# Performance work log

Measured on AMD Instinct MI355X. Metric: run time of the kernel, lower is better.

The kernel has to match this reference:

```python
import jax, jax.numpy as jnp
import numpy as np

W, H = 1920, 1080
WEIGHT = 0.2          # self.weight
CONT_W = 0.1          # continuity_weight
RANK_M = 1e-4         # ranking_margin
CONT_M = 1e-4         # continuity_margin
SAMPLE_RATIO = 0.25
R = 3                 # knn_crop_radius
PAD_VAL = -1000000.0


def setup_inputs() -> dict:
    key = jax.random.key(0)
    k1, k2, k3 = jax.random.split(key, 3)
    return {
        "target_depths": jax.random.uniform(k1, (1, H * W), dtype=jnp.float32) * 100.0,
        "render_depths": jax.random.uniform(k2, (H * W,), dtype=jnp.float32) * 100.0,
        "valid_mask": jax.random.randint(k3, (1, H * W, 1), 0, 2, dtype=jnp.int32),
        "width": W,
        "height": H,
    }


def _sample_depth_loss_indices(depths, width, height, valid_mask, n_samples,
                               rank_patch_size, r, key):
    win = 2 * r + 1                      # 7
    top_n = int(0.3 * win * win + 1)     # 15
    ks = jax.random.split(key, 5)
    sy = jax.random.randint(ks[0], (n_samples, 1), 0, height - rank_patch_size)
    sx = jax.random.randint(ks[1], (n_samples, 1), 0, width - rank_patch_size)
    sy = sy + jax.random.randint(ks[2], (n_samples, 2), 0, rank_patch_size)
    sx = sx + jax.random.randint(ks[3], (n_samples, 2), 0, rank_patch_size)
    sample_idx = sy * width + sx                               # (n, 2)
    sampled_depth = depths[0][sample_idx]                      # (n, 2)

    padded = jnp.pad(depths.reshape(height, width), r, constant_values=PAD_VAL)
    dy = jnp.repeat(jnp.arange(win), win)                      # (49,) row offsets
    dx = jnp.tile(jnp.arange(win), win)                        # (49,) col offsets
    # padded coords: (y - r + dy) + r == y + dy
    py = sy[..., None] + dy                                    # (n, 2, 49)
    px = sx[..., None] + dx
    depth_crops = padded[py, px]                               # (n, 2, 49)

    sorted_crop_idx = jnp.argsort(jnp.abs(depth_crops - sampled_depth[..., None]), axis=-1)
    nbr_sample = jax.random.randint(ks[4], (n_samples, 2, 1), 1, top_n)
    rel = jnp.take_along_axis(sorted_crop_idx, nbr_sample, axis=-1)[..., 0]  # (n, 2)
    ny = sy - r + rel // win
    nx = sx - r + rel % win
    neighbours_idx = ny * width + nx                           # (n, 2)

    vm = valid_mask[0].astype(bool)                            # (H*W, C)
    samples_mask = vm[sample_idx].any(-1).all(-1)              # (n,)
    neighbours_mask = vm[neighbours_idx].any(-1).all(-1)
    full_mask = samples_mask & neighbours_mask

    # per-pair descending sort by sampled target depth
    order = jnp.argsort(-sampled_depth, axis=-1)
    s_sorted = jnp.take_along_axis(sample_idx, order, axis=-1)
    n_sorted = jnp.take_along_axis(neighbours_idx, order, axis=-1)
    idx4 = jnp.concatenate([s_sorted, n_sorted], axis=-1)      # (n, 4)
    return idx4, full_mask


def reference(target_depths, render_depths, valid_mask, width, height):
    n_samples = int(width * height * SAMPLE_RATIO)
    rank_patch_size = width // 8
    idx4, mask = _sample_depth_loss_indices(
        target_depths, width, height, valid_mask, n_samples, rank_patch_size,
        R, jax.random.key(42))
    d = render_depths[idx4].reshape(-1, 2, 2)                  # (n, 2, 2)
    rank = jnp.maximum(d[:, 0, 0] - d[:, 0, 1] + RANK_M, 0.0)  # (n,)
    cont = jnp.maximum(jnp.abs(d[:, 0, :] - d[:, 1, :]) - CONT_M, 0.0)  # (n, 2)
    # masked means == torch's boolean filtering followed by .mean()
    m = mask.astype(rank.dtype)
    denom = jnp.maximum(m.sum(), 1.0)
    rank_mean = (rank * m).sum() / denom
    cont_mean = (cont * m[:, None]).sum() / (denom * 2.0)
    return jnp.stack([WEIGHT * rank_mean, WEIGHT * CONT_W * cont_mean])
```

## Files before the change

kernel.cpp:

```cpp
#include <hip/hip_runtime.h>
#include <stdint.h>


#define IMG_W 1920
#define IMG_H 1080
#define N_PIX (IMG_W * IMG_H)
#define N_SAMP 518400
#define PAD_VAL (-1000000.0f)

struct Keys { uint32_t k[5][2][2]; };

static __host__ __device__ inline void tf2x32(uint32_t k0, uint32_t k1,
                                              uint32_t x0, uint32_t x1,
                                              uint32_t& o0, uint32_t& o1)
{
  const uint32_t ks2 = k0 ^ k1 ^ 0x1BD11BDAu;
  x0 += k0; x1 += k1;
#define TFR(r) { x0 += x1; x1 = (x1 << (r)) | (x1 >> (32 - (r))); x1 ^= x0; }
  TFR(13) TFR(15) TFR(26) TFR(6)
  x0 += k1;  x1 += ks2 + 1u;
  TFR(17) TFR(29) TFR(16) TFR(24)
  x0 += ks2; x1 += k0 + 2u;
  TFR(13) TFR(15) TFR(26) TFR(6)
  x0 += k0;  x1 += k1 + 3u;
  TFR(17) TFR(29) TFR(16) TFR(24)
  x0 += k1;  x1 += ks2 + 4u;
  TFR(13) TFR(15) TFR(26) TFR(6)
  x0 += ks2; x1 += k0 + 5u;
#undef TFR
  o0 = x0; o1 = x1;
}

__device__ __forceinline__ uint32_t jrbits(const uint32_t kk[2], uint32_t f)
{
  uint32_t a, b;
  tf2x32(kk[0], kk[1], 0u, f, a, b);
  return a ^ b;
}

__device__ __forceinline__ uint32_t jrandint(const Keys& K, int r, uint32_t f,
                                             uint32_t span)
{
  const uint32_t hi = jrbits(K.k[r][0], f);
  const uint32_t lo = jrbits(K.k[r][1], f);
  uint32_t m = 65536u % span;
  m = (m * m) % span;
  return ((hi % span) * m + (lo % span)) % span;
}

static void compute_keys(Keys& K)
{
  uint32_t ks[5][2];
  for (uint32_t t = 0; t < 5; t++) {
    uint32_t a, b; tf2x32(0u, 42u, 0u, t, a, b);
    ks[t][0] = a; ks[t][1] = b;
  }
  for (int r = 0; r < 5; r++) {
    uint32_t a, b;
    tf2x32(ks[r][0], ks[r][1], 0u, 0u, a, b); K.k[r][0][0] = a; K.k[r][0][1] = b;
    tf2x32(ks[r][0], ks[r][1], 0u, 1u, a, b); K.k[r][1][0] = a; K.k[r][1][1] = b;
  }
}

__device__ __forceinline__ bool validat(const unsigned long long* __restrict__ vb,
                                        const int* __restrict__ vm, uint32_t idx)
{
  if (vb) return ((vb[idx >> 6] >> (idx & 63u)) & 1ull) != 0ull;
  return vm[idx] != 0;
}

__global__ __launch_bounds__(256) void gs_bitpack(
    const int* __restrict__ vmask,
    unsigned long long* __restrict__ vbits)
{
  const uint32_t gid = blockIdx.x * 256u + threadIdx.x;
  const unsigned long long ball = __ballot(vmask[gid] != 0);
  if ((threadIdx.x & 63u) == 0) vbits[gid >> 6] = ball;
}

__device__ __forceinline__ int crop_neighbor(const float* __restrict__ tgt,
                                             int sy, int sx, float sd,
                                             uint32_t nbr)
{
  float v[7][8];
  const bool interior = (sy >= 3) && (sy <= IMG_H - 4) &&
                        (sx >= 3) && (sx <= IMG_W - 5);
  if (interior) {
    const float* p = tgt + (sy - 3) * IMG_W + (sx - 3);
#pragma unroll
    for (int r = 0; r < 7; r++)
      __builtin_memcpy(&v[r][0], p + r * IMG_W, 32);
  } else {
#pragma unroll
    for (int r = 0; r < 7; r++) {
      const int yy = sy - 3 + r;
      const bool rok = (yy >= 0) && (yy < IMG_H);
#pragma unroll
      for (int c = 0; c < 8; c++) {
        const int xx = sx - 3 + c;
        const bool okc = rok && (c < 7) && (xx >= 0) && (xx < IMG_W);
        v[r][c] = okc ? tgt[yy * IMG_W + xx] : PAD_VAL;
      }
    }
  }
  __builtin_amdgcn_sched_barrier(0);

  uint32_t arr[15];
#pragma unroll
  for (int t = 0; t < 15; t++) arr[t] = 0xFFFFFFFFu;

#pragma unroll
  for (int r = 0; r < 7; r++) {
#pragma unroll
    for (int c = 0; c < 7; c++) {
      const int q = r * 7 + c;
      uint32_t key = (__float_as_uint(v[r][c] - sd) & 0x7FFFFFC0u) | (uint32_t)q;
      const int depth = (q + 1 < 15) ? (q + 1) : 15;
#pragma unroll
      for (int t = 0; t < 15; t++) {
        if (t < depth) {
          const uint32_t lo = min(key, arr[t]);
          const uint32_t hi = max(key, arr[t]);
          arr[t] = lo; key = hi;
        }
      }
    }
  }

  uint32_t relkey = 0;
#pragma unroll
  for (int t = 1; t < 15; t++)
    if ((uint32_t)t == nbr) relkey = arr[t];
  const uint32_t rel = relkey & 63u;
  const int ny = sy - 3 + (int)(rel / 7u);
  const int nx = sx - 3 + (int)(rel % 7u);
  return ny * IMG_W + nx;
}

__global__ __launch_bounds__(256, 2) void gs_fused(
    const float* __restrict__ tgt,
    const float* __restrict__ rnd,
    const int*   __restrict__ vmask,
    const unsigned long long* __restrict__ vbits,
    float* __restrict__ acc,
    Keys K)
{
  __shared__ unsigned long long ent[512];
  __shared__ float    res_sd[1024];
  __shared__ int      res_ni[1024];
  __shared__ uint32_t scnt[8];
  __shared__ float    partial[12];

  const uint32_t tid  = threadIdx.x;
  const uint32_t lane = tid & 63u;
  const uint32_t wave = tid >> 6;

  unsigned long long e[2];
  bool ok[2];
#pragma unroll
  for (int h = 0; h < 2; h++) {
    const uint32_t ui = blockIdx.x * 512u + (uint32_t)h * 256u + tid;
    bool o = false;
    unsigned long long ee = 0;
    if (ui < N_SAMP) {
      const uint32_t syb = jrandint(K, 0, ui, 840u);
      const uint32_t sxb = jrandint(K, 1, ui, 1680u);
      const uint32_t sy0 = syb + jrandint(K, 2, 2u * ui,      240u);
      const uint32_t sy1 = syb + jrandint(K, 2, 2u * ui + 1u, 240u);
      const uint32_t sx0 = sxb + jrandint(K, 3, 2u * ui,      240u);
      const uint32_t sx1 = sxb + jrandint(K, 3, 2u * ui + 1u, 240u);
      o = validat(vbits, vmask, sy0 * IMG_W + sx0) &&
          validat(vbits, vmask, sy1 * IMG_W + sx1);
      ee = ((unsigned long long)ui  << 44) |
           ((unsigned long long)sy0 << 33) | ((unsigned long long)sx0 << 22) |
           ((unsigned long long)sy1 << 11) |  (unsigned long long)sx1;
    }
    ok[h] = o; e[h] = ee;
  }

  const unsigned long long b0 = __ballot(ok[0]);
  const unsigned long long b1 = __ballot(ok[1]);
  if (lane == 0) {
    scnt[wave]     = (uint32_t)__popcll(b0);
    scnt[4 + wave] = (uint32_t)__popcll(b1);
  }
  __syncthreads();

  uint32_t base0 = 0, sum0 = 0, base1 = 0, nsurv = 0;
#pragma unroll
  for (uint32_t w = 0; w < 4; w++) {
    if (w < wave) { base0 += scnt[w]; base1 += scnt[4 + w]; }
    sum0  += scnt[w];
    nsurv += scnt[w] + scnt[4 + w];
  }
  base1 += sum0;

  if (ok[0]) ent[base0 + (uint32_t)__popcll(b0 & ((1ull << lane) - 1ull))] = e[0];
  if (ok[1]) ent[base1 + (uint32_t)__popcll(b1 & ((1ull << lane) - 1ull))] = e[1];
  __syncthreads();

  for (uint32_t t = tid; t < 2u * nsurv; t += 256u) {
    const unsigned long long ee = ent[t >> 1];
    const int jj = (int)(t & 1u);
    const uint32_t eui = (uint32_t)(ee >> 44);
    const int sy = jj ? (int)((ee >> 11) & 2047u) : (int)((ee >> 33) & 2047u);
    const int sx = jj ? (int)( ee        & 2047u) : (int)((ee >> 22) & 2047u);

    const float sd = tgt[sy * IMG_W + sx];
    const uint32_t nbr = 1u + jrandint(K, 4, 2u * eui + (uint32_t)jj, 14u);
    const int nidx = crop_neighbor(tgt, sy, sx, sd, nbr);
    res_sd[t] = sd;
    res_ni[t] = validat(vbits, vmask, (uint32_t)nidx) ? nidx : -1;
  }
  __syncthreads();

  float rank_c = 0.f, cont_c = 0.f, cnt_c = 0.f;
  for (uint32_t s = tid; s < nsurv; s += 256u) {
    const int n0 = res_ni[2u * s], n1 = res_ni[2u * s + 1u];
    if ((n0 >= 0) && (n1 >= 0)) {
      const unsigned long long ee = ent[s];
      const int esy0 = (int)((ee >> 33) & 2047u), esx0 = (int)((ee >> 22) & 2047u);
      const int esy1 = (int)((ee >> 11) & 2047u), esx1 = (int)( ee        & 2047u);
      const float r0 = rnd[esy0 * IMG_W + esx0];
      const float r1 = rnd[esy1 * IMG_W + esx1];
      const float q0 = rnd[n0], q1 = rnd[n1];
      const float sd0 = res_sd[2u * s], sd1 = res_sd[2u * s + 1u];
      const bool keep = sd0 >= sd1;
      const float ra = keep ? r0 : r1;
      const float rb = keep ? r1 : r0;
      rank_c += fmaxf(ra - rb + 1e-4f, 0.f);
      cont_c += fmaxf(fabsf(r0 - q0) - 1e-4f, 0.f)
              + fmaxf(fabsf(r1 - q1) - 1e-4f, 0.f);
      cnt_c  += 1.f;
    }
  }

#pragma unroll
  for (int off = 32; off > 0; off >>= 1) {
    rank_c += __shfl_down(rank_c, off);
    cont_c += __shfl_down(cont_c, off);
    cnt_c  += __shfl_down(cnt_c, off);
  }
  if (lane == 0) {
    partial[wave * 3 + 0] = rank_c;
    partial[wave * 3 + 1] = cont_c;
    partial[wave * 3 + 2] = cnt_c;
  }
  __syncthreads();
  if (tid < 3) {
    const float s = partial[tid] + partial[3 + tid] +
                    partial[6 + tid] + partial[9 + tid];
    atomicAdd(acc + tid, s);
  }
}

__global__ void gs_finalize(const float* __restrict__ acc, float* __restrict__ out)
{
  const float denom = fmaxf(acc[2], 1.0f);
  out[0] = 0.2f * (acc[0] / denom);
  out[1] = 0.2f * 0.1f * (acc[1] / (denom * 2.0f));
}

extern "C" void kernel_launch(void* const* d_in, const int* in_sizes, int n_in,
                              void* d_out, int out_size, void* d_ws, size_t ws_size,
                              hipStream_t stream)
{
  (void)in_sizes; (void)n_in; (void)out_size;
  const float* tgt   = (const float*)d_in[0];
  const float* rnd   = (const float*)d_in[1];
  const int*   vmask = (const int*)d_in[2];
  float* out = (float*)d_out;

  float* acc = (float*)d_ws;
  unsigned long long* vbits = (unsigned long long*)((char*)d_ws + 16);
  const size_t need = 16 + (size_t)(N_PIX / 64) * 8;

  Keys K;
  compute_keys(K);

  hipMemsetAsync(acc, 0, 16, stream);

  const bool use_bits = (ws_size >= need);
  if (use_bits)
    gs_bitpack<<<N_PIX / 256, 256, 0, stream>>>(vmask, vbits);

  const int blocksF = (N_SAMP + 511) / 512;
  gs_fused<<<blocksF, 256, 0, stream>>>(tgt, rnd, vmask,
                                        use_bits ? vbits : nullptr, acc, K);
  gs_finalize<<<1, 1, 0, stream>>>(acc, out);
}
```

Before: 60.42 us.

## Double samples per block and process two crop sorts per thread iteration

Each block now generates 1024 samples instead of 512, which halves the grid to 507 blocks and doubles the shared-memory compaction buffers. In the crop phase each thread handles two sample points per iteration with interleaved insertion sorts, which increases instruction-level parallelism and memory loads in flight. In exchange, register pressure rises (two 7x8 crops and two sort arrays per thread), with possible spills or lower occupancy. Fewer blocks may also under-fill the GPU and leave the tail iteration partially idle.

```diff
diff --git a/kernel.cpp b/kernel.cpp
--- a/kernel.cpp
+++ b/kernel.cpp
@@ -6,7 +6,10 @@
 #define IMG_H 1080
 #define N_PIX (IMG_W * IMG_H)
 #define N_SAMP 518400
+#define MAIN_BLKS 507
 #define PAD_VAL (-1000000.0f)
+
+typedef unsigned long long ull;
 
 struct Keys { uint32_t k[5][2][2]; };
 
@@ -62,7 +65,7 @@
   }
 }
 
-__device__ __forceinline__ bool validat(const unsigned long long* __restrict__ vb,
+__device__ __forceinline__ bool validat(const ull* __restrict__ vb,
                                         const int* __restrict__ vm, uint32_t idx)
 {
   if (vb) return ((vb[idx >> 6] >> (idx & 63u)) & 1ull) != 0ull;
@@ -71,160 +74,193 @@
 
 __global__ __launch_bounds__(256) void gs_bitpack(
     const int* __restrict__ vmask,
-    unsigned long long* __restrict__ vbits)
+    ull* __restrict__ vbits)
 {
   const uint32_t gid = blockIdx.x * 256u + threadIdx.x;
-  const unsigned long long ball = __ballot(vmask[gid] != 0);
+  const ull ball = __ballot(vmask[gid] != 0);
   if ((threadIdx.x & 63u) == 0) vbits[gid >> 6] = ball;
 }
 
-__device__ __forceinline__ int crop_neighbor(const float* __restrict__ tgt,
-                                             int sy, int sx, float sd,
-                                             uint32_t nbr)
-{
-  float v[7][8];
-  const bool interior = (sy >= 3) && (sy <= IMG_H - 4) &&
-                        (sx >= 3) && (sx <= IMG_W - 5);
-  if (interior) {
-    const float* p = tgt + (sy - 3) * IMG_W + (sx - 3);
-#pragma unroll
-    for (int r = 0; r < 7; r++)
-      __builtin_memcpy(&v[r][0], p + r * IMG_W, 32);
-  } else {
-#pragma unroll
-    for (int r = 0; r < 7; r++) {
-      const int yy = sy - 3 + r;
-      const bool rok = (yy >= 0) && (yy < IMG_H);
-#pragma unroll
-      for (int c = 0; c < 8; c++) {
-        const int xx = sx - 3 + c;
-        const bool okc = rok && (c < 7) && (xx >= 0) && (xx < IMG_W);
-        v[r][c] = okc ? tgt[yy * IMG_W + xx] : PAD_VAL;
+__device__ __forceinline__ void crop_pair(
+    const float* __restrict__ tgt,
+    const int* sy, const int* sx, const float* sd,
+    const uint32_t* nbr, int* nidx)
+{
+  float v[2][7][8];
+#pragma unroll
+  for (int k = 0; k < 2; k++) {
+    const bool interior = (sy[k] >= 3) && (sy[k] <= IMG_H - 4) &&
+                          (sx[k] >= 3) && (sx[k] <= IMG_W - 5);
+    if (interior) {
+      const float* p = tgt + (sy[k] - 3) * IMG_W + (sx[k] - 3);
+#pragma unroll
+      for (int r = 0; r < 7; r++)
+        __builtin_memcpy(&v[k][r][0], p + r * IMG_W, 32);
+    } else {
+#pragma unroll
+      for (int r = 0; r < 7; r++) {
+        const int yy = sy[k] - 3 + r;
+        const bool rok = (yy >= 0) && (yy < IMG_H);
+#pragma unroll
+        for (int c = 0; c < 8; c++) {
+          const int xx = sx[k] - 3 + c;
+          const bool okc = rok && (c < 7) && (xx >= 0) && (xx < IMG_W);
+          v[k][r][c] = okc ? tgt[yy * IMG_W + xx] : PAD_VAL;
+        }
       }
     }
   }
-  __builtin_amdgcn_sched_barrier(0);
-
-  uint32_t arr[15];
-#pragma unroll
-  for (int t = 0; t < 15; t++) arr[t] = 0xFFFFFFFFu;
+
+  uint32_t arr[2][15];
+#pragma unroll
+  for (int k = 0; k < 2; k++)
+#pragma unroll
+    for (int t = 0; t < 15; t++) arr[k][t] = 0xFFFFFFFFu;
 
 #pragma unroll
   for (int r = 0; r < 7; r++) {
 #pragma unroll
     for (int c = 0; c < 7; c++) {
       const int q = r * 7 + c;
-      uint32_t key = (__float_as_uint(v[r][c] - sd) & 0x7FFFFFC0u) | (uint32_t)q;
       const int depth = (q + 1 < 15) ? (q + 1) : 15;
 #pragma unroll
-      for (int t = 0; t < 15; t++) {
-        if (t < depth) {
-          const uint32_t lo = min(key, arr[t]);
-          const uint32_t hi = max(key, arr[t]);
-          arr[t] = lo; key = hi;
+      for (int k = 0; k < 2; k++) {
+        uint32_t key = (__float_as_uint(v[k][r][c] - sd[k]) & 0x7FFFFFC0u)
+                     | (uint32_t)q;
+#pragma unroll
+        for (int t = 0; t < 15; t++) {
+          if (t < depth) {
+            const uint32_t lo = min(key, arr[k][t]);
+            const uint32_t hi = max(key, arr[k][t]);
+            arr[k][t] = lo; key = hi;
+          }
         }
       }
     }
   }
 
-  uint32_t relkey = 0;
-#pragma unroll
-  for (int t = 1; t < 15; t++)
-    if ((uint32_t)t == nbr) relkey = arr[t];
-  const uint32_t rel = relkey & 63u;
-  const int ny = sy - 3 + (int)(rel / 7u);
-  const int nx = sx - 3 + (int)(rel % 7u);
-  return ny * IMG_W + nx;
+#pragma unroll
+  for (int k = 0; k < 2; k++) {
+    uint32_t relkey = 0;
+#pragma unroll
+    for (int t = 1; t < 15; t++)
+      if ((uint32_t)t == nbr[k]) relkey = arr[k][t];
+    const uint32_t rel = relkey & 63u;
+    nidx[k] = (sy[k] - 3 + (int)(rel / 7u)) * IMG_W
+            + (sx[k] - 3 + (int)(rel % 7u));
+  }
 }
 
 __global__ __launch_bounds__(256, 2) void gs_fused(
     const float* __restrict__ tgt,
     const float* __restrict__ rnd,
     const int*   __restrict__ vmask,
-    const unsigned long long* __restrict__ vbits,
+    const ull*   __restrict__ vbits,
     float* __restrict__ acc,
     Keys K)
 {
-  __shared__ unsigned long long ent[512];
-  __shared__ float    res_sd[1024];
-  __shared__ int      res_ni[1024];
-  __shared__ uint32_t scnt[8];
+  __shared__ ull      ent[1024];
+  __shared__ float    res_sd[2048];
+  __shared__ int      res_ni[2048];
+  __shared__ uint32_t scnt[16];
   __shared__ float    partial[12];
 
   const uint32_t tid  = threadIdx.x;
   const uint32_t lane = tid & 63u;
   const uint32_t wave = tid >> 6;
 
-  unsigned long long e[2];
-  bool ok[2];
-#pragma unroll
-  for (int h = 0; h < 2; h++) {
-    const uint32_t ui = blockIdx.x * 512u + (uint32_t)h * 256u + tid;
+  ull  eb[4];
+  ull  bal[4];
+  bool ok[4];
+#pragma unroll
+  for (int h = 0; h < 4; h++) {
+    const uint32_t ui = blockIdx.x * 1024u + (uint32_t)h * 256u + tid;
     bool o = false;
-    unsigned long long ee = 0;
+    ull ee = 0;
     if (ui < N_SAMP) {
       const uint32_t syb = jrandint(K, 0, ui, 840u);
       const uint32_t sxb = jrandint(K, 1, ui, 1680u);
-      const uint32_t sy0 = syb + jrandint(K, 2, 2u * ui,      240u);
-      const uint32_t sy1 = syb + jrandint(K, 2, 2u * ui + 1u, 240u);
-      const uint32_t sx0 = sxb + jrandint(K, 3, 2u * ui,      240u);
-      const uint32_t sx1 = sxb + jrandint(K, 3, 2u * ui + 1u, 240u);
+      const uint32_t oy0 = jrandint(K, 2, 2u * ui,      240u);
+      const uint32_t oy1 = jrandint(K, 2, 2u * ui + 1u, 240u);
+      const uint32_t ox0 = jrandint(K, 3, 2u * ui,      240u);
+      const uint32_t ox1 = jrandint(K, 3, 2u * ui + 1u, 240u);
+      const uint32_t sy0 = syb + oy0, sy1 = syb + oy1;
+      const uint32_t sx0 = sxb + ox0, sx1 = sxb + ox1;
       o = validat(vbits, vmask, sy0 * IMG_W + sx0) &&
           validat(vbits, vmask, sy1 * IMG_W + sx1);
-      ee = ((unsigned long long)ui  << 44) |
-           ((unsigned long long)sy0 << 33) | ((unsigned long long)sx0 << 22) |
-           ((unsigned long long)sy1 << 11) |  (unsigned long long)sx1;
-    }
-    ok[h] = o; e[h] = ee;
-  }
-
-  const unsigned long long b0 = __ballot(ok[0]);
-  const unsigned long long b1 = __ballot(ok[1]);
-  if (lane == 0) {
-    scnt[wave]     = (uint32_t)__popcll(b0);
-    scnt[4 + wave] = (uint32_t)__popcll(b1);
+      ee = ((ull)ui << 44) |
+           ((ull)sy0 << 33) | ((ull)sx0 << 22) |
+           ((ull)sy1 << 11) |  (ull)sx1;
+    }
+    ok[h] = o; eb[h] = ee;
+    bal[h] = __ballot(o);
+    if (lane == 0) scnt[(uint32_t)h * 4u + wave] = (uint32_t)__popcll(bal[h]);
   }
   __syncthreads();
 
-  uint32_t base0 = 0, sum0 = 0, base1 = 0, nsurv = 0;
-#pragma unroll
-  for (uint32_t w = 0; w < 4; w++) {
-    if (w < wave) { base0 += scnt[w]; base1 += scnt[4 + w]; }
-    sum0  += scnt[w];
-    nsurv += scnt[w] + scnt[4 + w];
-  }
-  base1 += sum0;
-
-  if (ok[0]) ent[base0 + (uint32_t)__popcll(b0 & ((1ull << lane) - 1ull))] = e[0];
-  if (ok[1]) ent[base1 + (uint32_t)__popcll(b1 & ((1ull << lane) - 1ull))] = e[1];
+  uint32_t run = 0, baseh[4];
+#pragma unroll
+  for (uint32_t h = 0; h < 4; h++) {
+    uint32_t b = run;
+#pragma unroll
+    for (uint32_t w = 0; w < 4; w++) {
+      const uint32_t cwh = scnt[h * 4u + w];
+      if (w < wave) b += cwh;
+      run += cwh;
+    }
+    baseh[h] = b;
+  }
+  const uint32_t nsurv = run;
+
+#pragma unroll
+  for (int h = 0; h < 4; h++)
+    if (ok[h])
+      ent[baseh[h] + (uint32_t)__popcll(bal[h] & ((1ull << lane) - 1ull))] = eb[h];
   __syncthreads();
 
-  for (uint32_t t = tid; t < 2u * nsurv; t += 256u) {
-    const unsigned long long ee = ent[t >> 1];
-    const int jj = (int)(t & 1u);
-    const uint32_t eui = (uint32_t)(ee >> 44);
-    const int sy = jj ? (int)((ee >> 11) & 2047u) : (int)((ee >> 33) & 2047u);
-    const int sx = jj ? (int)( ee        & 2047u) : (int)((ee >> 22) & 2047u);
-
-    const float sd = tgt[sy * IMG_W + sx];
-    const uint32_t nbr = 1u + jrandint(K, 4, 2u * eui + (uint32_t)jj, 14u);
-    const int nidx = crop_neighbor(tgt, sy, sx, sd, nbr);
-    res_sd[t] = sd;
-    res_ni[t] = validat(vbits, vmask, (uint32_t)nidx) ? nidx : -1;
+  const uint32_t m = 2u * nsurv;
+  for (uint32_t t0 = tid; t0 < m; t0 += 512u) {
+    const uint32_t tA = t0;
+    const uint32_t tB = t0 + 256u;
+    const bool hasB = (tB < m);
+    const uint32_t tt[2] = { tA, hasB ? tB : tA };
+
+    int sy[2], sx[2], nidx[2];
+    uint32_t nbr[2];
+    float sd[2];
+#pragma unroll
+    for (int k = 0; k < 2; k++) {
+      const ull ee = ent[tt[k] >> 1];
+      const int jj = (int)(tt[k] & 1u);
+      const uint32_t eui = (uint32_t)(ee >> 44);
+      sy[k] = jj ? (int)((ee >> 11) & 2047u) : (int)((ee >> 33) & 2047u);
+      sx[k] = jj ? (int)( ee        & 2047u) : (int)((ee >> 22) & 2047u);
+      nbr[k] = 1u + jrandint(K, 4, 2u * eui + (uint32_t)jj, 14u);
+      sd[k] = tgt[sy[k] * IMG_W + sx[k]];
+    }
+
+    crop_pair(tgt, sy, sx, sd, nbr, nidx);
+
+    res_sd[tA] = sd[0];
+    res_ni[tA] = validat(vbits, vmask, (uint32_t)nidx[0]) ? nidx[0] : -1;
+    if (hasB) {
+      res_sd[tB] = sd[1];
+      res_ni[tB] = validat(vbits, vmask, (uint32_t)nidx[1]) ? nidx[1] : -1;
+    }
   }
   __syncthreads();
 
   float rank_c = 0.f, cont_c = 0.f, cnt_c = 0.f;
-  for (uint32_t s = tid; s < nsurv; s += 256u) {
-    const int n0 = res_ni[2u * s], n1 = res_ni[2u * s + 1u];
+  for (uint32_t sI = tid; sI < nsurv; sI += 256u) {
+    const int n0 = res_ni[2u * sI], n1 = res_ni[2u * sI + 1u];
     if ((n0 >= 0) && (n1 >= 0)) {
-      const unsigned long long ee = ent[s];
+      const ull ee = ent[sI];
       const int esy0 = (int)((ee >> 33) & 2047u), esx0 = (int)((ee >> 22) & 2047u);
       const int esy1 = (int)((ee >> 11) & 2047u), esx1 = (int)( ee        & 2047u);
       const float r0 = rnd[esy0 * IMG_W + esx0];
       const float r1 = rnd[esy1 * IMG_W + esx1];
       const float q0 = rnd[n0], q1 = rnd[n1];
-      const float sd0 = res_sd[2u * s], sd1 = res_sd[2u * s + 1u];
+      const float sd0 = res_sd[2u * sI], sd1 = res_sd[2u * sI + 1u];
       const bool keep = sd0 >= sd1;
       const float ra = keep ? r0 : r1;
       const float rb = keep ? r1 : r0;
@@ -257,8 +293,8 @@
 __global__ void gs_finalize(const float* __restrict__ acc, float* __restrict__ out)
 {
   const float denom = fmaxf(acc[2], 1.0f);
-  out[0] = 0.2f * (acc[0] / denom);
-  out[1] = 0.2f * 0.1f * (acc[1] / (denom * 2.0f));
+  out[0] = 0.2f  * (acc[0] / denom);
+  out[1] = 0.02f * (acc[1] / (denom * 2.0f));
 }
 
 extern "C" void kernel_launch(void* const* d_in, const int* in_sizes, int n_in,
@@ -271,8 +307,8 @@
   const int*   vmask = (const int*)d_in[2];
   float* out = (float*)d_out;
 
-  float* acc = (float*)d_ws;
-  unsigned long long* vbits = (unsigned long long*)((char*)d_ws + 16);
+  float* acc  = (float*)d_ws;
+  ull*   vbits = (ull*)((char*)d_ws + 16);
   const size_t need = 16 + (size_t)(N_PIX / 64) * 8;
 
   Keys K;
@@ -284,8 +320,7 @@
   if (use_bits)
     gs_bitpack<<<N_PIX / 256, 256, 0, stream>>>(vmask, vbits);
 
-  const int blocksF = (N_SAMP + 511) / 512;
-  gs_fused<<<blocksF, 256, 0, stream>>>(tgt, rnd, vmask,
-                                        use_bits ? vbits : nullptr, acc, K);
+  gs_fused<<<MAIN_BLKS, 256, 0, stream>>>(tgt, rnd, vmask,
+                                          use_bits ? vbits : nullptr, acc, K);
   gs_finalize<<<1, 1, 0, stream>>>(acc, out);
 }
```

Result: slower. 65.67 us (+8.7%).
